# Kernel tuning notes

Measured on AMD Instinct MI355X. Metric: run time of the kernel, lower is better.

Reference implementation:

```python
import jax, jax.numpy as jnp
import numpy as np

N_NODES = 20000
N_EDGES = 100000
WIDTH = 64
KER_IN = 6
KER_HID = WIDTH // 4  # 16
DEPTH = 6


def setup_inputs() -> dict:
    key = jax.random.key(0)
    ks = jax.random.split(key, 12)
    s = lambda fan_in: 1.0 / np.sqrt(fan_in)
    return {
        "x": jax.random.normal(ks[0], (N_NODES, 1), dtype=jnp.float32),
        "edge_index": jax.random.randint(ks[1], (2, N_EDGES), 0, N_NODES, dtype=jnp.int32),
        "edge_attr": jax.random.uniform(ks[2], (N_EDGES, KER_IN), dtype=jnp.float32),
        "fc1_w": jax.random.normal(ks[3], (1, WIDTH), dtype=jnp.float32) * s(1),
        "fc1_b": jnp.zeros((WIDTH,), dtype=jnp.float32),
        "k1_w": jax.random.normal(ks[4], (KER_IN, KER_HID), dtype=jnp.float32) * s(KER_IN),
        "k1_b": jnp.zeros((KER_HID,), dtype=jnp.float32),
        "k2_w": jax.random.normal(ks[5], (KER_HID, WIDTH * WIDTH), dtype=jnp.float32) * s(KER_HID),
        "k2_b": jnp.zeros((WIDTH * WIDTH,), dtype=jnp.float32),
        "root_w": jax.random.normal(ks[6], (WIDTH, WIDTH), dtype=jnp.float32) * s(WIDTH),
        "conv_b": jnp.zeros((WIDTH,), dtype=jnp.float32),
        "fc2_w": jax.random.normal(ks[7], (WIDTH, 1), dtype=jnp.float32) * s(WIDTH),
        "fc2_b": jnp.zeros((1,), dtype=jnp.float32),
    }


def reference(x, edge_index, edge_attr, fc1_w, fc1_b, k1_w, k1_b, k2_w, k2_b,
              root_w, conv_b, fc2_w, fc2_b):
    src = edge_index[0]  # source nodes j
    dst = edge_index[1]  # target nodes i

    # fc1: lift node features [N,1] -> [N,W]
    h = x @ fc1_w + fc1_b

    # Edge-conditioned weight matrices via kernel MLP (edge_attr is layer-invariant,
    # so compute once and reuse for all DEPTH layers — identical math).
    ek = jax.nn.relu(edge_attr @ k1_w + k1_b)           # [E, W/4]
    W = (ek @ k2_w + k2_b).reshape(N_EDGES, WIDTH, WIDTH)  # [E, W, W]

    # mean aggregation denominator (in-degree, clamped to avoid div-by-zero)
    deg = jax.ops.segment_sum(jnp.ones((N_EDGES,), dtype=h.dtype), dst,
                              num_segments=N_NODES)
    denom = jnp.maximum(deg, 1.0)[:, None]               # [N,1]

    for _ in range(DEPTH):
        # per-edge matmul: msg_e = x_src[e] @ W_e
        msg = jnp.einsum('ei,eio->eo', h[src], W)        # [E, W]
        agg = jax.ops.segment_sum(msg, dst, num_segments=N_NODES) / denom
        h = jax.nn.relu(agg + h @ root_w + conv_b)       # NNConv root weight + bias, then outer ReLU

    return h @ fc2_w + fc2_b                              # [N, 1]
```

## Files before the change

### kernel.cpp

```cpp
#include <hip/hip_runtime.h>
#include <hip/hip_bf16.h>


#define NN 20000
#define NE 100000
#define WD 64
#define DEPTH 6
#define TM 15
#define LSTR 1092

typedef __attribute__((ext_vector_type(8))) short bf16x8;
typedef __attribute__((ext_vector_type(4))) float f32x4;

__device__ __forceinline__ unsigned short f2bf(float v) {
    union { float f; unsigned u; } x; x.f = v;
    unsigned r = x.u + 0x7fffu + ((x.u >> 16) & 1u);
    return (unsigned short)(r >> 16);
}
__device__ __forceinline__ float bf2f(unsigned short b) {
    union { unsigned u; float f; } x; x.u = ((unsigned)b) << 16;
    return x.f;
}

__global__ __launch_bounds__(256) void count_kernel(const int* __restrict__ ei,
                                                    int* __restrict__ outc,
                                                    int* __restrict__ inc)
{
    int e = blockIdx.x * 256 + threadIdx.x;
    if (e >= NE) return;
    atomicAdd(&outc[ei[e]], 1);
    atomicAdd(&inc[ei[NE + e]], 1);
}

__global__ __launch_bounds__(256) void scanA_kernel(const int* __restrict__ cnt,
                                                    int* __restrict__ partials)
{
    int b = blockIdx.x, t = threadIdx.x, lane = t & 63, w = t >> 6;
    int base = b * 1024 + t * 4;
    int s = 0;
#pragma unroll
    for (int i = 0; i < 4; ++i) {
        int idx = base + i;
        if (idx < 2 * NN) s += cnt[idx];
    }
#pragma unroll
    for (int off = 32; off > 0; off >>= 1) s += __shfl_down(s, off, 64);
    __shared__ int wsum[4];
    if (lane == 0) wsum[w] = s;
    __syncthreads();
    if (t == 0) partials[b] = wsum[0] + wsum[1] + wsum[2] + wsum[3];
}

__global__ __launch_bounds__(64) void scanB_kernel(const int* __restrict__ partials,
                                                   int* __restrict__ bases)
{
    int l = threadIdx.x;
    int p = (l < 40) ? partials[l] : 0;
    int v = p;
#pragma unroll
    for (int off = 1; off < 64; off <<= 1) {
        int u = __shfl_up(v, off, 64);
        if (l >= off) v += u;
    }
    if (l < 40) bases[l] = v - p;
}

__global__ __launch_bounds__(256) void scanC_kernel(const int* __restrict__ cnt,
                                                    const int* __restrict__ bases,
                                                    int* __restrict__ rps,
                                                    int* __restrict__ rpd,
                                                    float* __restrict__ invd)
{
    int b = blockIdx.x, t = threadIdx.x, lane = t & 63, w = t >> 6;
    int base = b * 1024 + t * 4;
    int v[4], s = 0;
#pragma unroll
    for (int i = 0; i < 4; ++i) {
        int idx = base + i;
        v[i] = (idx < 2 * NN) ? cnt[idx] : 0;
        s += v[i];
    }
    int tsum = s, sc = s;
#pragma unroll
    for (int off = 1; off < 64; off <<= 1) {
        int u = __shfl_up(sc, off, 64);
        if (lane >= off) sc += u;
    }
    __shared__ int wtot[4];
    if (lane == 63) wtot[w] = sc;
    __syncthreads();
    int wbase = 0;
    for (int j = 0; j < w; ++j) wbase += wtot[j];
    int run = bases[b] + wbase + sc - tsum;
#pragma unroll
    for (int i = 0; i < 4; ++i) {
        int idx = base + i;
        int e = run; run += v[i];
        if (idx < NN) {
            rps[idx] = e;
        } else if (idx < 2 * NN) {
            rpd[idx - NN] = e - NE;
            invd[idx - NN] = 1.0f / fmaxf((float)v[i], 1.0f);
        }
    }
    if (b == 0 && t == 0) { rps[NN] = NE; rpd[NN] = NE; }
}

__global__ __launch_bounds__(256) void ekfill_kernel(
    const int* __restrict__ ei, const float* __restrict__ ea,
    const float* __restrict__ k1w, const float* __restrict__ k1b,
    const int* __restrict__ rps, const int* __restrict__ rpd,
    int* __restrict__ fs, int* __restrict__ fd,
    float* __restrict__ eks, int* __restrict__ ss2sd)
{
    int e = blockIdx.x * 256 + threadIdx.x;
    if (e >= NE) return;
    int s = ei[e], d = ei[NE + e];
    float a[6];
#pragma unroll
    for (int i = 0; i < 6; ++i) a[i] = ea[e * 6 + i];
    int slot_s = rps[s] + atomicAdd(&fs[s], 1);
    int slot_d = rpd[d] + atomicAdd(&fd[d], 1);
    ss2sd[slot_s] = slot_d;
#pragma unroll
    for (int j = 0; j < 16; ++j) {
        float v = k1b[j];
#pragma unroll
        for (int i = 0; i < 6; ++i) v = fmaf(a[i], k1w[i * 16 + j], v);
        eks[(size_t)slot_s * 16 + j] = fmaxf(v, 0.f);
    }
}

__global__ __launch_bounds__(256) void gwt_kernel(
    const float* __restrict__ k2w, const float* __restrict__ k2b,
    const float* __restrict__ rootw,
    unsigned short* __restrict__ Gh, unsigned short* __restrict__ Gl)
{
    int idx = blockIdx.x * 256 + threadIdx.x;
    if (idx >= 1152 * 64) return;
    int n = idx >> 6, k = idx & 63;
    int b = n >> 6, o = n & 63;
    float g;
    if (b < 16)       g = k2w[b * 4096 + k * 64 + o];
    else if (b == 16) g = k2b[k * 64 + o];
    else              g = rootw[k * 64 + o];
    unsigned short hi = f2bf(g);
    Gh[idx] = hi;
    Gl[idx] = f2bf(g - bf2f(hi));
}

__global__ __launch_bounds__(256) void h0_kernel(
    const float* __restrict__ x, const float* __restrict__ w,
    const float* __restrict__ b,
    unsigned short* __restrict__ hhi, unsigned short* __restrict__ hlo)
{
    int idx = blockIdx.x * 256 + threadIdx.x;
    if (idx >= NN * WD) return;
    int n = idx >> 6, o = idx & 63;
    float v = fmaf(x[n], w[o], b[o]);
    unsigned short hi = f2bf(v);
    hhi[idx] = hi;
    hlo[idx] = f2bf(v - bf2f(hi));
}

__global__ __launch_bounds__(512) void fused_kernel(
    const unsigned short* __restrict__ hhi, const unsigned short* __restrict__ hlo,
    const unsigned short* __restrict__ Gh, const unsigned short* __restrict__ Gl,
    const float* __restrict__ eks, const int* __restrict__ ss2sd,
    const int* __restrict__ rps, float* __restrict__ Proot,
    float* __restrict__ msg)
{
    __shared__ __align__(16) float Pt[TM * LSTR];
    __shared__ int rb[TM + 1];
    int n0 = blockIdx.x * TM;
    int w = threadIdx.x >> 6, l = threadIdx.x & 63;
    int quad = l >> 4, lr = l & 15;
    if (threadIdx.x < TM + 1) {
        int gi = n0 + threadIdx.x;
        rb[threadIdx.x] = rps[gi > NN ? NN : gi];
    }
    int arow = n0 + lr;
    if (arow > NN - 1) arow = NN - 1;
    const bf16x8* pah = (const bf16x8*)(hhi + (size_t)arow * 64 + quad * 8);
    const bf16x8* pal = (const bf16x8*)(hlo + (size_t)arow * 64 + quad * 8);
    bf16x8 ah0 = pah[0], ah1 = pah[4];
    bf16x8 al0 = pal[0], al1 = pal[4];

    for (int st = w; st < 18; st += 8) {
        f32x4 acc[4];
#pragma unroll
        for (int t = 0; t < 4; ++t) acc[t] = (f32x4){0.f, 0.f, 0.f, 0.f};
#pragma unroll
        for (int t = 0; t < 4; ++t) {
            int brow = st * 64 + t * 16 + lr;
            const bf16x8* pbh = (const bf16x8*)(Gh + (size_t)brow * 64 + quad * 8);
            const bf16x8* pbl = (const bf16x8*)(Gl + (size_t)brow * 64 + quad * 8);
            bf16x8 bh0 = pbh[0], bh1 = pbh[4];
            bf16x8 bl0 = pbl[0], bl1 = pbl[4];
            f32x4 a = acc[t];
            a = __builtin_amdgcn_mfma_f32_16x16x32_bf16(ah0, bh0, a, 0, 0, 0);
            a = __builtin_amdgcn_mfma_f32_16x16x32_bf16(ah0, bl0, a, 0, 0, 0);
            a = __builtin_amdgcn_mfma_f32_16x16x32_bf16(al0, bh0, a, 0, 0, 0);
            a = __builtin_amdgcn_mfma_f32_16x16x32_bf16(ah1, bh1, a, 0, 0, 0);
            a = __builtin_amdgcn_mfma_f32_16x16x32_bf16(ah1, bl1, a, 0, 0, 0);
            a = __builtin_amdgcn_mfma_f32_16x16x32_bf16(al1, bh1, a, 0, 0, 0);
            acc[t] = a;
        }
        if (st < 17) {
#pragma unroll
            for (int t = 0; t < 4; ++t)
#pragma unroll
                for (int r = 0; r < 4; ++r) {
                    int row = quad * 4 + r;
                    if (row < TM)
                        Pt[row * LSTR + st * 64 + t * 16 + lr] = acc[t][r];
                }
        } else {
#pragma unroll
            for (int t = 0; t < 4; ++t)
#pragma unroll
                for (int r = 0; r < 4; ++r) {
                    int row = quad * 4 + r;
                    int gn = n0 + row;
                    if (row < TM && gn < NN)
                        Proot[(size_t)gn * 64 + t * 16 + lr] = acc[t][r];
                }
        }
    }
    __syncthreads();

    int nend = n0 + TM; if (nend > NN) nend = NN;
    int r0 = rb[0], r1 = rb[nend - n0];
    int total = r1 - r0;
    if (total <= 0) return;
    int per = (total + 7) >> 3;
    int s0 = r0 + w * per;
    int s1 = s0 + per; if (s1 > r1) s1 = r1;
    int ln = 0;
    float p[17];
    bool need = true;
    for (int s = s0; s < s1; ++s) {
        while (s >= rb[ln + 1]) { ++ln; need = true; }
        if (need) {
            const float* Pr = &Pt[ln * LSTR];
#pragma unroll
            for (int k = 0; k < 17; ++k) p[k] = Pr[k * 64 + l];
            need = false;
        }
        int su = __builtin_amdgcn_readfirstlane(s);
        const float* er = eks + (size_t)su * 16;
        f32x4 e0 = *(const f32x4*)(er);
        f32x4 e1 = *(const f32x4*)(er + 4);
        f32x4 e2 = *(const f32x4*)(er + 8);
        f32x4 e3 = *(const f32x4*)(er + 12);
        int ds = ss2sd[su];
        float ma = p[16], mb = 0.f;
        ma = fmaf(e0[0], p[0], ma);  mb = fmaf(e0[1], p[1], mb);
        ma = fmaf(e0[2], p[2], ma);  mb = fmaf(e0[3], p[3], mb);
        ma = fmaf(e1[0], p[4], ma);  mb = fmaf(e1[1], p[5], mb);
        ma = fmaf(e1[2], p[6], ma);  mb = fmaf(e1[3], p[7], mb);
        ma = fmaf(e2[0], p[8], ma);  mb = fmaf(e2[1], p[9], mb);
        ma = fmaf(e2[2], p[10], ma); mb = fmaf(e2[3], p[11], mb);
        ma = fmaf(e3[0], p[12], ma); mb = fmaf(e3[1], p[13], mb);
        ma = fmaf(e3[2], p[14], ma); mb = fmaf(e3[3], p[15], mb);
        msg[(size_t)ds * 64 + l] = ma + mb;
    }
}

__global__ __launch_bounds__(256) void agg_kernel(
    const float* __restrict__ msg, const int* __restrict__ rpd,
    const float* __restrict__ invd, const float* __restrict__ Proot,
    const float* __restrict__ convb, float* __restrict__ h,
    unsigned short* __restrict__ hhi, unsigned short* __restrict__ hlo)
{
    int i = blockIdx.x * 4 + (threadIdx.x >> 6);
    if (i >= NN) return;
    int l = threadIdx.x & 63;
    int r0 = rpd[i], r1 = rpd[i + 1];
    float a0 = 0.f, a1 = 0.f, a2 = 0.f, a3 = 0.f;
    int s = r0;
    for (; s + 3 < r1; s += 4) {
        a0 += msg[(size_t)s * 64 + l];
        a1 += msg[(size_t)(s + 1) * 64 + l];
        a2 += msg[(size_t)(s + 2) * 64 + l];
        a3 += msg[(size_t)(s + 3) * 64 + l];
    }
    for (; s < r1; ++s) a0 += msg[(size_t)s * 64 + l];
    float acc = (a0 + a1) + (a2 + a3);
    float v = fmaf(acc, invd[i], Proot[(size_t)i * 64 + l] + convb[l]);
    v = fmaxf(v, 0.f);
    int idx = i * 64 + l;
    h[idx] = v;
    unsigned short hi = f2bf(v);
    hhi[idx] = hi;
    hlo[idx] = f2bf(v - bf2f(hi));
}

__global__ __launch_bounds__(256) void out_kernel(
    const float* __restrict__ h, const float* __restrict__ fc2_w,
    const float* __restrict__ fc2_b, float* __restrict__ out)
{
    int wave = blockIdx.x * 4 + (threadIdx.x >> 6);
    int lane = threadIdx.x & 63;
    float v = h[(size_t)wave * 64 + lane] * fc2_w[lane];
#pragma unroll
    for (int off = 32; off > 0; off >>= 1) v += __shfl_down(v, off);
    if (lane == 0) out[wave] = v + fc2_b[0];
}

extern "C" void kernel_launch(void* const* d_in, const int* in_sizes, int n_in,
                              void* d_out, int out_size, void* d_ws, size_t ws_size,
                              hipStream_t stream)
{
    const float* x         = (const float*)d_in[0];
    const int*   ei        = (const int*)  d_in[1];
    const float* edge_attr = (const float*)d_in[2];
    const float* fc1_w     = (const float*)d_in[3];
    const float* fc1_b     = (const float*)d_in[4];
    const float* k1_w      = (const float*)d_in[5];
    const float* k1_b      = (const float*)d_in[6];
    const float* k2_w      = (const float*)d_in[7];
    const float* k2_b      = (const float*)d_in[8];
    const float* root_w    = (const float*)d_in[9];
    const float* conv_b    = (const float*)d_in[10];
    const float* fc2_w     = (const float*)d_in[11];
    const float* fc2_b     = (const float*)d_in[12];
    float* out = (float*)d_out;

    float* ws = (float*)d_ws;
    size_t off = 0;
    int* cnt   = (int*)(ws + off); off += 4 * NN;
    int* outc  = cnt;
    int* inc   = cnt + NN;
    int* fs    = cnt + 2 * NN;
    int* fd    = cnt + 3 * NN;
    int* rps   = (int*)(ws + off); off += 20004;
    int* rpd   = (int*)(ws + off); off += 20004;
    int* partials = (int*)(ws + off); off += 64;
    int* bases    = (int*)(ws + off); off += 64;
    int* ss2sd    = (int*)(ws + off); off += NE;
    float* invd  = ws + off; off += NN;
    float* eks   = ws + off; off += (size_t)NE * 16;
    unsigned short* Gh  = (unsigned short*)(ws + off); off += 36864;
    unsigned short* Gl  = (unsigned short*)(ws + off); off += 36864;
    unsigned short* hhi = (unsigned short*)(ws + off); off += (size_t)NN * 32;
    unsigned short* hlo = (unsigned short*)(ws + off); off += (size_t)NN * 32;
    float* h     = ws + off; off += (size_t)NN * WD;
    float* msg   = ws + off; off += (size_t)NE * WD;
    float* Proot = ws + off; off += (size_t)NN * WD;

    hipMemsetAsync(cnt, 0, 4 * NN * sizeof(int), stream);
    count_kernel<<<(NE + 255) / 256, 256, 0, stream>>>(ei, outc, inc);
    scanA_kernel<<<40, 256, 0, stream>>>(cnt, partials);
    scanB_kernel<<<1, 64, 0, stream>>>(partials, bases);
    scanC_kernel<<<40, 256, 0, stream>>>(cnt, bases, rps, rpd, invd);
    ekfill_kernel<<<(NE + 255) / 256, 256, 0, stream>>>(ei, edge_attr, k1_w, k1_b,
                                                        rps, rpd, fs, fd, eks, ss2sd);
    gwt_kernel<<<(1152 * 64 + 255) / 256, 256, 0, stream>>>(k2_w, k2_b, root_w, Gh, Gl);
    h0_kernel<<<(NN * WD + 255) / 256, 256, 0, stream>>>(x, fc1_w, fc1_b, hhi, hlo);

    int ntiles = (NN + TM - 1) / TM;
    for (int layer = 0; layer < DEPTH; ++layer) {
        fused_kernel<<<ntiles, 512, 0, stream>>>(hhi, hlo, Gh, Gl, eks, ss2sd,
                                                 rps, Proot, msg);
        agg_kernel<<<(NN + 3) / 4, 256, 0, stream>>>(msg, rpd, invd, Proot,
                                                     conv_b, h, hhi, hlo);
    }

    out_kernel<<<NN / 4, 256, 0, stream>>>(h, fc2_w, fc2_b, out);
}
```

Measured before the change: 561.5 us.

## Prefetch next edge data in fused kernel and shrink node tile

```diff
diff --git a/kernel.cpp b/kernel.cpp
--- a/kernel.cpp
+++ b/kernel.cpp
@@ -6,7 +6,7 @@
 #define NE 100000
 #define WD 64
 #define DEPTH 6
-#define TM 15
+#define TM 12
 #define LSTR 1092
 
 typedef __attribute__((ext_vector_type(8))) short bf16x8;
@@ -111,7 +111,7 @@
     const float* __restrict__ k1w, const float* __restrict__ k1b,
     const int* __restrict__ rps, const int* __restrict__ rpd,
     int* __restrict__ fs, int* __restrict__ fd,
-    float* __restrict__ eks, int* __restrict__ ss2sd)
+    float* __restrict__ eks, int* __restrict__ sdmeta)
 {
     int e = blockIdx.x * 256 + threadIdx.x;
     if (e >= NE) return;
@@ -121,7 +121,8 @@
     for (int i = 0; i < 6; ++i) a[i] = ea[e * 6 + i];
     int slot_s = rps[s] + atomicAdd(&fs[s], 1);
     int slot_d = rpd[d] + atomicAdd(&fd[d], 1);
-    ss2sd[slot_s] = slot_d;
+    sdmeta[2 * slot_s]     = slot_d;
+    sdmeta[2 * slot_s + 1] = s;
 #pragma unroll
     for (int j = 0; j < 16; ++j) {
         float v = k1b[j];
@@ -163,10 +164,10 @@
     hlo[idx] = f2bf(v - bf2f(hi));
 }
 
-__global__ __launch_bounds__(512) void fused_kernel(
+__global__ __launch_bounds__(512, 6) void fused_kernel(
     const unsigned short* __restrict__ hhi, const unsigned short* __restrict__ hlo,
     const unsigned short* __restrict__ Gh, const unsigned short* __restrict__ Gl,
-    const float* __restrict__ eks, const int* __restrict__ ss2sd,
+    const float* __restrict__ eks, const int* __restrict__ sdmeta,
     const int* __restrict__ rps, float* __restrict__ Proot,
     float* __restrict__ msg)
 {
@@ -236,34 +237,48 @@
     int per = (total + 7) >> 3;
     int s0 = r0 + w * per;
     int s1 = s0 + per; if (s1 > r1) s1 = r1;
-    int ln = 0;
+    if (s0 >= s1) return;
+
     float p[17];
-    bool need = true;
+    int lnp = -1;
+    int su = __builtin_amdgcn_readfirstlane(s0);
+    const float* er = eks + (size_t)su * 16;
+    f32x4 e0 = *(const f32x4*)(er);
+    f32x4 e1 = *(const f32x4*)(er + 4);
+    f32x4 e2 = *(const f32x4*)(er + 8);
+    f32x4 e3 = *(const f32x4*)(er + 12);
+    int ds  = sdmeta[2 * su];
+    int src = sdmeta[2 * su + 1];
+
     for (int s = s0; s < s1; ++s) {
-        while (s >= rb[ln + 1]) { ++ln; need = true; }
-        if (need) {
-            const float* Pr = &Pt[ln * LSTR];
+        f32x4 c0 = e0, c1 = e1, c2 = e2, c3 = e3;
+        int cds = ds, cln = src - n0;
+        if (s + 1 < s1) {
+            int su2 = __builtin_amdgcn_readfirstlane(s + 1);
+            const float* er2 = eks + (size_t)su2 * 16;
+            e0 = *(const f32x4*)(er2);
+            e1 = *(const f32x4*)(er2 + 4);
+            e2 = *(const f32x4*)(er2 + 8);
+            e3 = *(const f32x4*)(er2 + 12);
+            ds  = sdmeta[2 * su2];
+            src = sdmeta[2 * su2 + 1];
+        }
+        if (cln != lnp) {
+            const float* Pr = &Pt[cln * LSTR];
 #pragma unroll
             for (int k = 0; k < 17; ++k) p[k] = Pr[k * 64 + l];
-            need = false;
-        }
-        int su = __builtin_amdgcn_readfirstlane(s);
-        const float* er = eks + (size_t)su * 16;
-        f32x4 e0 = *(const f32x4*)(er);
-        f32x4 e1 = *(const f32x4*)(er + 4);
-        f32x4 e2 = *(const f32x4*)(er + 8);
-        f32x4 e3 = *(const f32x4*)(er + 12);
-        int ds = ss2sd[su];
+            lnp = cln;
+        }
         float ma = p[16], mb = 0.f;
-        ma = fmaf(e0[0], p[0], ma);  mb = fmaf(e0[1], p[1], mb);
-        ma = fmaf(e0[2], p[2], ma);  mb = fmaf(e0[3], p[3], mb);
-        ma = fmaf(e1[0], p[4], ma);  mb = fmaf(e1[1], p[5], mb);
-        ma = fmaf(e1[2], p[6], ma);  mb = fmaf(e1[3], p[7], mb);
-        ma = fmaf(e2[0], p[8], ma);  mb = fmaf(e2[1], p[9], mb);
-        ma = fmaf(e2[2], p[10], ma); mb = fmaf(e2[3], p[11], mb);
-        ma = fmaf(e3[0], p[12], ma); mb = fmaf(e3[1], p[13], mb);
-        ma = fmaf(e3[2], p[14], ma); mb = fmaf(e3[3], p[15], mb);
-        msg[(size_t)ds * 64 + l] = ma + mb;
+        ma = fmaf(c0[0], p[0], ma);  mb = fmaf(c0[1], p[1], mb);
+        ma = fmaf(c0[2], p[2], ma);  mb = fmaf(c0[3], p[3], mb);
+        ma = fmaf(c1[0], p[4], ma);  mb = fmaf(c1[1], p[5], mb);
+        ma = fmaf(c1[2], p[6], ma);  mb = fmaf(c1[3], p[7], mb);
+        ma = fmaf(c2[0], p[8], ma);  mb = fmaf(c2[1], p[9], mb);
+        ma = fmaf(c2[2], p[10], ma); mb = fmaf(c2[3], p[11], mb);
+        ma = fmaf(c3[0], p[12], ma); mb = fmaf(c3[1], p[13], mb);
+        ma = fmaf(c3[2], p[14], ma); mb = fmaf(c3[3], p[15], mb);
+        msg[(size_t)cds * 64 + l] = ma + mb;
     }
 }
 
@@ -338,7 +353,7 @@
     int* rpd   = (int*)(ws + off); off += 20004;
     int* partials = (int*)(ws + off); off += 64;
     int* bases    = (int*)(ws + off); off += 64;
-    int* ss2sd    = (int*)(ws + off); off += NE;
+    int* sdmeta   = (int*)(ws + off); off += 2 * NE + 16;
     float* invd  = ws + off; off += NN;
     float* eks   = ws + off; off += (size_t)NE * 16;
     unsigned short* Gh  = (unsigned short*)(ws + off); off += 36864;
@@ -355,13 +370,13 @@
     scanB_kernel<<<1, 64, 0, stream>>>(partials, bases);
     scanC_kernel<<<40, 256, 0, stream>>>(cnt, bases, rps, rpd, invd);
     ekfill_kernel<<<(NE + 255) / 256, 256, 0, stream>>>(ei, edge_attr, k1_w, k1_b,
-                                                        rps, rpd, fs, fd, eks, ss2sd);
+                                                        rps, rpd, fs, fd, eks, sdmeta);
     gwt_kernel<<<(1152 * 64 + 255) / 256, 256, 0, stream>>>(k2_w, k2_b, root_w, Gh, Gl);
     h0_kernel<<<(NN * WD + 255) / 256, 256, 0, stream>>>(x, fc1_w, fc1_b, hhi, hlo);
 
     int ntiles = (NN + TM - 1) / TM;
     for (int layer = 0; layer < DEPTH; ++layer) {
-        fused_kernel<<<ntiles, 512, 0, stream>>>(hhi, hlo, Gh, Gl, eks, ss2sd,
+        fused_kernel<<<ntiles, 512, 0, stream>>>(hhi, hlo, Gh, Gl, eks, sdmeta,
                                                  rps, Proot, msg);
         agg_kernel<<<(NN + 3) / 4, 256, 0, stream>>>(msg, rpd, invd, Proot,
                                                      conv_b, h, hhi, hlo);
```

After: 597.4 us. +6.4%, slower.

## Prefetch per-tile edge kernels and metadata into LDS before the MFMA phase

Applied to the files above, without the earlier changes.

```diff
diff --git a/kernel.cpp b/kernel.cpp
--- a/kernel.cpp
+++ b/kernel.cpp
@@ -8,6 +8,7 @@
 #define DEPTH 6
 #define TM 15
 #define LSTR 1092
+#define ECAP 192
 
 typedef __attribute__((ext_vector_type(8))) short bf16x8;
 typedef __attribute__((ext_vector_type(4))) float f32x4;
@@ -111,7 +112,7 @@
     const float* __restrict__ k1w, const float* __restrict__ k1b,
     const int* __restrict__ rps, const int* __restrict__ rpd,
     int* __restrict__ fs, int* __restrict__ fd,
-    float* __restrict__ eks, int* __restrict__ ss2sd)
+    float* __restrict__ eks, int* __restrict__ sdmeta)
 {
     int e = blockIdx.x * 256 + threadIdx.x;
     if (e >= NE) return;
@@ -121,7 +122,8 @@
     for (int i = 0; i < 6; ++i) a[i] = ea[e * 6 + i];
     int slot_s = rps[s] + atomicAdd(&fs[s], 1);
     int slot_d = rpd[d] + atomicAdd(&fd[d], 1);
-    ss2sd[slot_s] = slot_d;
+    sdmeta[2 * slot_s]     = slot_d;
+    sdmeta[2 * slot_s + 1] = s;
 #pragma unroll
     for (int j = 0; j < 16; ++j) {
         float v = k1b[j];
@@ -163,22 +165,37 @@
     hlo[idx] = f2bf(v - bf2f(hi));
 }
 
-__global__ __launch_bounds__(512) void fused_kernel(
+__global__ __launch_bounds__(512, 4) void fused_kernel(
     const unsigned short* __restrict__ hhi, const unsigned short* __restrict__ hlo,
     const unsigned short* __restrict__ Gh, const unsigned short* __restrict__ Gl,
-    const float* __restrict__ eks, const int* __restrict__ ss2sd,
+    const float* __restrict__ eks, const int* __restrict__ sdmeta,
     const int* __restrict__ rps, float* __restrict__ Proot,
     float* __restrict__ msg)
 {
     __shared__ __align__(16) float Pt[TM * LSTR];
-    __shared__ int rb[TM + 1];
+    __shared__ __align__(16) float eksT[ECAP * 16];
+    __shared__ __align__(8)  int   metaT[ECAP * 2];
     int n0 = blockIdx.x * TM;
-    int w = threadIdx.x >> 6, l = threadIdx.x & 63;
+    int tid = threadIdx.x;
+    int w = tid >> 6, l = tid & 63;
     int quad = l >> 4, lr = l & 15;
-    if (threadIdx.x < TM + 1) {
-        int gi = n0 + threadIdx.x;
-        rb[threadIdx.x] = rps[gi > NN ? NN : gi];
-    }
+
+    int nend = n0 + TM; if (nend > NN) nend = NN;
+    int r0 = rps[n0];
+    int r1 = rps[nend];
+    int total = r1 - r0;
+    int nst = total > ECAP ? ECAP : total;
+    int nw = nst * 16;
+
+    bool v0 = tid * 4 < nw;
+    bool v1 = 2048 + tid * 4 < nw;
+    bool vm = tid < nst;
+    f32x4 st0 = {0.f, 0.f, 0.f, 0.f}, st1 = {0.f, 0.f, 0.f, 0.f};
+    int2 mv = {0, 0};
+    if (v0) st0 = *(const f32x4*)(eks + (size_t)r0 * 16 + tid * 4);
+    if (v1) st1 = *(const f32x4*)(eks + (size_t)r0 * 16 + 2048 + tid * 4);
+    if (vm) mv  = ((const int2*)sdmeta)[r0 + tid];
+
     int arow = n0 + lr;
     if (arow > NN - 1) arow = NN - 1;
     const bf16x8* pah = (const bf16x8*)(hhi + (size_t)arow * 64 + quad * 8);
@@ -227,33 +244,42 @@
                 }
         }
     }
+
+    if (v0) *(f32x4*)&eksT[tid * 4] = st0;
+    if (v1) *(f32x4*)&eksT[2048 + tid * 4] = st1;
+    if (vm) ((int2*)metaT)[tid] = mv;
     __syncthreads();
 
-    int nend = n0 + TM; if (nend > NN) nend = NN;
-    int r0 = rb[0], r1 = rb[nend - n0];
-    int total = r1 - r0;
     if (total <= 0) return;
     int per = (total + 7) >> 3;
-    int s0 = r0 + w * per;
-    int s1 = s0 + per; if (s1 > r1) s1 = r1;
-    int ln = 0;
+    int j0 = w * per;
+    int j1 = j0 + per; if (j1 > total) j1 = total;
     float p[17];
-    bool need = true;
-    for (int s = s0; s < s1; ++s) {
-        while (s >= rb[ln + 1]) { ++ln; need = true; }
-        if (need) {
-            const float* Pr = &Pt[ln * LSTR];
+    int lnp = -1;
+    for (int j = j0; j < j1; ++j) {
+        f32x4 e0, e1, e2, e3;
+        int ds, src;
+        if (j < ECAP) {
+            const f32x4* eb = (const f32x4*)&eksT[j * 16];
+            e0 = eb[0]; e1 = eb[1]; e2 = eb[2]; e3 = eb[3];
+            int2 m = ((const int2*)metaT)[j];
+            ds = m.x; src = m.y;
+        } else {
+            const float* er = eks + (size_t)(r0 + j) * 16;
+            e0 = *(const f32x4*)(er);
+            e1 = *(const f32x4*)(er + 4);
+            e2 = *(const f32x4*)(er + 8);
+            e3 = *(const f32x4*)(er + 12);
+            int2 m = ((const int2*)sdmeta)[r0 + j];
+            ds = m.x; src = m.y;
+        }
+        int cln = src - n0;
+        if (cln != lnp) {
+            const float* Pr = &Pt[cln * LSTR];
 #pragma unroll
             for (int k = 0; k < 17; ++k) p[k] = Pr[k * 64 + l];
-            need = false;
-        }
-        int su = __builtin_amdgcn_readfirstlane(s);
-        const float* er = eks + (size_t)su * 16;
-        f32x4 e0 = *(const f32x4*)(er);
-        f32x4 e1 = *(const f32x4*)(er + 4);
-        f32x4 e2 = *(const f32x4*)(er + 8);
-        f32x4 e3 = *(const f32x4*)(er + 12);
-        int ds = ss2sd[su];
+            lnp = cln;
+        }
         float ma = p[16], mb = 0.f;
         ma = fmaf(e0[0], p[0], ma);  mb = fmaf(e0[1], p[1], mb);
         ma = fmaf(e0[2], p[2], ma);  mb = fmaf(e0[3], p[3], mb);
@@ -338,7 +364,7 @@
     int* rpd   = (int*)(ws + off); off += 20004;
     int* partials = (int*)(ws + off); off += 64;
     int* bases    = (int*)(ws + off); off += 64;
-    int* ss2sd    = (int*)(ws + off); off += NE;
+    int* sdmeta   = (int*)(ws + off); off += 2 * NE + 16;
     float* invd  = ws + off; off += NN;
     float* eks   = ws + off; off += (size_t)NE * 16;
     unsigned short* Gh  = (unsigned short*)(ws + off); off += 36864;
@@ -355,13 +381,13 @@
     scanB_kernel<<<1, 64, 0, stream>>>(partials, bases);
     scanC_kernel<<<40, 256, 0, stream>>>(cnt, bases, rps, rpd, invd);
     ekfill_kernel<<<(NE + 255) / 256, 256, 0, stream>>>(ei, edge_attr, k1_w, k1_b,
-                                                        rps, rpd, fs, fd, eks, ss2sd);
+                                                        rps, rpd, fs, fd, eks, sdmeta);
     gwt_kernel<<<(1152 * 64 + 255) / 256, 256, 0, stream>>>(k2_w, k2_b, root_w, Gh, Gl);
     h0_kernel<<<(NN * WD + 255) / 256, 256, 0, stream>>>(x, fc1_w, fc1_b, hhi, hlo);
 
     int ntiles = (NN + TM - 1) / TM;
     for (int layer = 0; layer < DEPTH; ++layer) {
-        fused_kernel<<<ntiles, 512, 0, stream>>>(hhi, hlo, Gh, Gl, eks, ss2sd,
+        fused_kernel<<<ntiles, 512, 0, stream>>>(hhi, hlo, Gh, Gl, eks, sdmeta,
                                                  rps, Proot, msg);
         agg_kernel<<<(NN + 3) / 4, 256, 0, stream>>>(msg, rpd, invd, Proot,
                                                      conv_b, h, hhi, hlo);
```

Measured after the change: 630.4 us. +12.3%, slower.
